# Performance work log

Measured on AMD Instinct MI355X. Metric: run time of the kernel, lower is better.

The kernel has to match this reference:

```python
import jax, jax.numpy as jnp
import numpy as np

EPS = 1e-6

def setup_inputs() -> dict:
    key = jax.random.key(0)
    ks = jax.random.split(key, 8)
    I, S, O = 1024, 512, 1024
    Bsz, T = 4, 2048
    return {
        "u": jax.random.normal(ks[0], (Bsz, T, I), dtype=jnp.float32),
        "dt": jax.random.normal(ks[1], (S,), dtype=jnp.float32),
        "A": jax.random.normal(ks[2], (S,), dtype=jnp.float32),
        "Bmat": jax.random.normal(ks[3], (I, S), dtype=jnp.float32) / np.sqrt(S),
        "C": jax.random.normal(ks[4], (S, O), dtype=jnp.float32) / np.sqrt(S),
        "D": jax.random.normal(ks[5], (O,), dtype=jnp.float32),
        "norm_w": jnp.ones((I,), dtype=jnp.float32),
    }

def _rmsnorm(x, w):
    x32 = x.astype(jnp.float32)
    n = x32 * jax.lax.rsqrt(jnp.mean(x32 * x32, axis=-1, keepdims=True) + EPS)
    return n.astype(x.dtype) * w

def reference(u, dt, A, Bmat, C, D, norm_w):
    u = _rmsnorm(u, norm_w)                      # [B, T, I]
    Bsz, T, _ = u.shape
    dts = jax.nn.sigmoid(dt)                     # [S]
    a = jnp.exp(-dts * jnp.abs(A))               # [S] discretized decay
    t = jnp.arange(T, dtype=jnp.float32)
    h = dts[:, None] * a[:, None] ** t[None, :]  # [S, T] geometric kernel
    u_proj = jnp.einsum('bti,is->bst', u, Bmat)  # [B, S, T]
    # depthwise causal conv: flipped kernel + cross-correlation == convolution
    k = jnp.flip(h, axis=1)[:, None, :]          # [S, 1, T] (OIW)
    x = jax.lax.conv_general_dilated(
        u_proj, k, window_strides=(1,), padding=[(T - 1, T - 1)],
        dimension_numbers=('NCW', 'OIW', 'NCW'),
        feature_group_count=u_proj.shape[1])[:, :, :T]  # [B, S, T]
    x = jnp.transpose(x, (0, 2, 1))              # [B, T, S]
    y = jnp.einsum('bts,so->bto', x, C) + D      # [B, T, O]
    return (y, x[:, -1])
```

## Files before the change

### kernel.cpp

```cpp
#include <hip/hip_runtime.h>
#include <math.h>

#define I_DIM 1024
#define S_DIM 512
#define O_DIM 1024
#define T_DIM 2048
#define B_SZ 4
#define M_ROWS (B_SZ * T_DIM)
#define EPSF 1e-6f

#define CL 64
#define NCH 32

typedef _Float16 f16;
typedef __attribute__((ext_vector_type(8))) _Float16 f16x8;
typedef __attribute__((ext_vector_type(2))) _Float16 f16x2;
typedef __attribute__((ext_vector_type(4))) float f32x4;

__device__ __forceinline__ unsigned short f2h_bits(float f) {
    _Float16 h = (_Float16)f;
    return __builtin_bit_cast(unsigned short, h);
}

__device__ __forceinline__ void load16_lds(const void* g, void* l) {
    __builtin_amdgcn_global_load_lds((const __attribute__((address_space(1))) void*)g,
                                     (__attribute__((address_space(3))) void*)l,
                                     16, 0, 0);
}

__global__ __launch_bounds__(256)
void prep(const float* __restrict__ u, const float* __restrict__ nw,
          unsigned short* __restrict__ u16,
          const float* __restrict__ Bmat, const float* __restrict__ dt,
          unsigned short* __restrict__ Bt16,
          const float* __restrict__ Cmat, unsigned short* __restrict__ Ct16) {
    __shared__ float tile[32][33];
    const int t = threadIdx.x;
    const int bx = blockIdx.x;

    if (bx < M_ROWS) {
        float4 v = ((const float4*)(u + (size_t)bx * I_DIM))[t];
        float ss = v.x * v.x + v.y * v.y + v.z * v.z + v.w * v.w;
        #pragma unroll
        for (int off = 32; off > 0; off >>= 1) ss += __shfl_down(ss, off, 64);
        if ((t & 63) == 0) tile[0][t >> 6] = ss;
        __syncthreads();
        if (t == 0)
            tile[0][0] = rsqrtf((tile[0][0] + tile[0][1] + tile[0][2] + tile[0][3])
                                * (1.0f / I_DIM) + EPSF);
        __syncthreads();
        const float rs = tile[0][0];
        ushort4 o;
        o.x = f2h_bits(v.x * rs);
        o.y = f2h_bits(v.y * rs);
        o.z = f2h_bits(v.z * rs);
        o.w = f2h_bits(v.w * rs);
        ((ushort4*)(u16 + (size_t)bx * I_DIM))[t] = o;
    } else if (bx < M_ROWS + 512) {
        const int tb = bx - M_ROWS;
        const int bs = (tb & 15) * 32;
        const int bi = (tb >> 4) * 32;
        const int tx = t & 31, ty = t >> 5;
        #pragma unroll
        for (int i = ty; i < 32; i += 8)
            tile[i][tx] = Bmat[(size_t)(bi + i) * S_DIM + bs + tx];
        __syncthreads();
        const float w = nw[bi + tx];
        #pragma unroll
        for (int i = ty; i < 32; i += 8) {
            const int s = bs + i;
            const float dts = 1.0f / (1.0f + expf(-dt[s]));
            Bt16[(size_t)s * I_DIM + bi + tx] = f2h_bits(tile[tx][i] * dts * w);
        }
    } else {
        const int tb = bx - M_ROWS - 512;
        const int bo = (tb & 31) * 32;
        const int bs = (tb >> 5) * 32;
        const int tx = t & 31, ty = t >> 5;
        #pragma unroll
        for (int i = ty; i < 32; i += 8)
            tile[i][tx] = Cmat[(size_t)(bs + i) * O_DIM + bo + tx];
        __syncthreads();
        #pragma unroll
        for (int i = ty; i < 32; i += 8)
            Ct16[(size_t)(bo + i) * S_DIM + bs + tx] = f2h_bits(tile[tx][i]);
    }
}

__global__ __launch_bounds__(256)
void gemm1_chfin(const f16* __restrict__ A, const f16* __restrict__ Bt,
                 f16* __restrict__ up, float* __restrict__ chlast,
                 const float* __restrict__ dt, const float* __restrict__ Avec) {
    constexpr int K = I_DIM, N = S_DIM, NK = K / 32;
    __shared__ f16 As[5][64 * 32];
    __shared__ f16 Bs[5][128 * 32];
    const int t = threadIdx.x;

    int bid = blockIdx.x;
    bid = (bid & 7) * 64 + (bid >> 3);
    const int n0 = (bid & 3) * 128;
    const int m0 = (bid >> 2) * 64;
    const int wid = t >> 6, lane = t & 63;
    const int wn = wid * 32, lr = lane & 15, kg = lane >> 4;

    const int swch = (t & 3) ^ ((t >> 3) & 3);
    const f16* aptr = A + (size_t)(m0 + (t >> 2)) * K + swch * 8;
    const f16* bptr = Bt + (size_t)(n0 + (t >> 2)) * K + swch * 8;
    const int rchunk = (kg ^ ((lr >> 1) & 3)) * 8;

    f32x4 acc[4][2];
    #pragma unroll
    for (int i = 0; i < 4; ++i)
        #pragma unroll
        for (int j = 0; j < 2; ++j) acc[i][j] = (f32x4){0.f, 0.f, 0.f, 0.f};

    auto stage = [&](int kt, int slot) {
        load16_lds(aptr + kt * 32, &As[slot][t * 8]);
        load16_lds(bptr + kt * 32, &Bs[slot][t * 8]);
        load16_lds(bptr + (size_t)64 * K + kt * 32, &Bs[slot][2048 + t * 8]);
    };

    stage(0, 0); stage(1, 1); stage(2, 2); stage(3, 3);

    #pragma unroll
    for (int kt = 0; kt < NK; ++kt) {
        if (kt < NK - 3)       asm volatile("s_waitcnt vmcnt(9)");
        else if (kt == NK - 3) asm volatile("s_waitcnt vmcnt(6)");
        else if (kt == NK - 2) asm volatile("s_waitcnt vmcnt(3)");
        else                   asm volatile("s_waitcnt vmcnt(0)");
        __builtin_amdgcn_s_barrier();
        __builtin_amdgcn_sched_barrier(0);
        if (kt + 4 < NK) stage(kt + 4, (kt + 4) % 5);

        const int slot = kt % 5;
        f16x8 af[4], bf[2];
        #pragma unroll
        for (int m = 0; m < 4; ++m)
            af[m] = *(const f16x8*)&As[slot][(m * 16 + lr) * 32 + rchunk];
        #pragma unroll
        for (int n = 0; n < 2; ++n)
            bf[n] = *(const f16x8*)&Bs[slot][(wn + n * 16 + lr) * 32 + rchunk];
        __builtin_amdgcn_s_setprio(1);
        #pragma unroll
        for (int m = 0; m < 4; ++m)
            #pragma unroll
            for (int n = 0; n < 2; ++n)
                acc[m][n] = __builtin_amdgcn_mfma_f32_16x16x32_f16(af[m], bf[n], acc[m][n], 0, 0, 0);
        __builtin_amdgcn_s_setprio(0);
    }

    const int cb = m0 >> 11;
    const int cc = (m0 >> 6) & (NCH - 1);
    #pragma unroll
    for (int n = 0; n < 2; ++n) {
        const int col = n0 + wn + n * 16 + lr;
        const float dts = 1.0f / (1.0f + expf(-dt[col]));
        const float e = dts * fabsf(Avec[col]);
        const float ainv = expf(e);
        float partial = 0.f;
        #pragma unroll
        for (int m = 0; m < 4; ++m) {
            const int row = m * 16 + kg * 4;
            float wgt = expf(-e * (float)(63 - row));
            #pragma unroll
            for (int j = 0; j < 4; ++j) {
                const float val = acc[m][n][j];
                up[(size_t)(m0 + row + j) * N + col] = (_Float16)val;
                partial = fmaf(wgt, val, partial);
                wgt *= ainv;
            }
        }
        partial += __shfl_xor(partial, 16, 64);
        partial += __shfl_xor(partial, 32, 64);
        if (kg == 0)
            chlast[(size_t)(cb * NCH + cc) * S_DIM + col] = partial;
    }
}

__global__ __launch_bounds__(256)
void gemm2_scan(const f16* __restrict__ upb, const float* __restrict__ chlast,
                const f16* __restrict__ Ct, const float* __restrict__ Dvec,
                const float* __restrict__ dt, const float* __restrict__ Avec,
                float* __restrict__ y, float* __restrict__ xlast) {
    constexpr int K = S_DIM, N = O_DIM, NK = K / 32;
    __shared__ __align__(16) unsigned char As[64 * 1024];
    __shared__ f16 Bs[2][128 * 32];
    const int t = threadIdx.x;

    int bid = blockIdx.x;
    bid = (bid & 7) * 128 + (bid >> 3);
    const int n0 = (bid & 7) * 128;
    const int m0 = (bid >> 3) * 64;
    const int wid = t >> 6, lane = t & 63;
    const int wn = wid * 32, lr = lane & 15, kg = lane >> 4;

    const int srcswz = ((t & 3) ^ ((t >> 3) & 3)) * 8;
    const f16* bptr = Ct + (size_t)(n0 + (t >> 2)) * K + srcswz;
    auto stageB = [&](int kt, int slot) {
        load16_lds(bptr + kt * 32, &Bs[slot][t * 8]);
        load16_lds(bptr + (size_t)64 * K + kt * 32, &Bs[slot][2048 + t * 8]);
    };
    stageB(0, 0);
    const int rchunk = (kg ^ ((lr >> 1) & 3)) * 8;

    const unsigned* up32 = (const unsigned*)upb;
    const size_t ub = (size_t)m0 * 256 + t;
    unsigned v[CL];
    #pragma unroll
    for (int j = 0; j < CL; ++j) v[j] = up32[ub + (size_t)j * 256];

    const int cc = (m0 >> 6) & (NCH - 1);
    const int cb = m0 >> 11;
    const int s0 = 2 * t;
    const float dts0 = 1.0f / (1.0f + expf(-dt[s0]));
    const float dts1 = 1.0f / (1.0f + expf(-dt[s0 + 1]));
    const float ab0 = fabsf(Avec[s0]), ab1 = fabsf(Avec[s0 + 1]);
    const float g0 = expf(-dts0 * ab0);
    const float g1 = expf(-dts1 * ab1);
    const float gCL0 = expf(-dts0 * ab0 * (float)CL);
    const float gCL1 = expf(-dts1 * ab1 * (float)CL);
    const float2* ch = (const float2*)chlast;
    float cy0 = 0.f, cy1 = 0.f;
    {
        int j = 0;
        for (; j + 4 <= cc; j += 4) {
            float2 f0 = ch[(size_t)(cb * NCH + j + 0) * 256 + t];
            float2 f1 = ch[(size_t)(cb * NCH + j + 1) * 256 + t];
            float2 f2 = ch[(size_t)(cb * NCH + j + 2) * 256 + t];
            float2 f3 = ch[(size_t)(cb * NCH + j + 3) * 256 + t];
            cy0 = fmaf(gCL0, cy0, f0.x); cy1 = fmaf(gCL1, cy1, f0.y);
            cy0 = fmaf(gCL0, cy0, f1.x); cy1 = fmaf(gCL1, cy1, f1.y);
            cy0 = fmaf(gCL0, cy0, f2.x); cy1 = fmaf(gCL1, cy1, f2.y);
            cy0 = fmaf(gCL0, cy0, f3.x); cy1 = fmaf(gCL1, cy1, f3.y);
        }
        for (; j < cc; ++j) {
            float2 f = ch[(size_t)(cb * NCH + j) * 256 + t];
            cy0 = fmaf(gCL0, cy0, f.x);
            cy1 = fmaf(gCL1, cy1, f.y);
        }
    }

    float x0 = cy0, x1 = cy1;
    #pragma unroll
    for (int j = 0; j < CL; ++j) {
        f16x2 h = __builtin_bit_cast(f16x2, v[j]);
        x0 = fmaf(g0, x0, (float)h.x);
        x1 = fmaf(g1, x1, (float)h.y);
        f16x2 o; o.x = (_Float16)x0; o.y = (_Float16)x1;
        v[j] = __builtin_bit_cast(unsigned, o);
    }
    #pragma unroll
    for (int j = 0; j < CL; ++j)
        *(unsigned*)&As[j * 1024 + ((t * 4) ^ ((j & 7) << 4))] = v[j];
    if (cc == NCH - 1)
        ((float2*)xlast)[cb * 256 + t] = make_float2(x0, x1);
    __syncthreads();

    f32x4 acc[4][2];
    #pragma unroll
    for (int i = 0; i < 4; ++i)
        #pragma unroll
        for (int j = 0; j < 2; ++j) acc[i][j] = (f32x4){0.f, 0.f, 0.f, 0.f};

    const int swz = (lr & 7) << 4;
    for (int kt = 0; kt < NK; ++kt) {
        const int cur = kt & 1;
        if (kt + 1 < NK) {
            stageB(kt + 1, cur ^ 1);
            asm volatile("s_waitcnt vmcnt(2)");
        } else {
            asm volatile("s_waitcnt vmcnt(0)");
        }
        __builtin_amdgcn_s_barrier();
        __builtin_amdgcn_sched_barrier(0);

        f16x8 af[4], bf[2];
        #pragma unroll
        for (int m = 0; m < 4; ++m)
            af[m] = *(const f16x8*)&As[(m * 16 + lr) * 1024 + ((kt * 64 + kg * 16) ^ swz)];
        #pragma unroll
        for (int n = 0; n < 2; ++n)
            bf[n] = *(const f16x8*)&Bs[cur][(wn + n * 16 + lr) * 32 + rchunk];
        __builtin_amdgcn_s_setprio(1);
        #pragma unroll
        for (int m = 0; m < 4; ++m)
            #pragma unroll
            for (int n = 0; n < 2; ++n)
                acc[m][n] = __builtin_amdgcn_mfma_f32_16x16x32_f16(af[m], bf[n], acc[m][n], 0, 0, 0);
        __builtin_amdgcn_s_setprio(0);
        __builtin_amdgcn_s_barrier();
    }

    #pragma unroll
    for (int n = 0; n < 2; ++n) {
        const int col = n0 + wn + n * 16 + lr;
        const float dv = Dvec[col];
        #pragma unroll
        for (int m = 0; m < 4; ++m) {
            const int row = m0 + m * 16 + kg * 4;
            #pragma unroll
            for (int j = 0; j < 4; ++j)
                y[(size_t)(row + j) * N + col] = acc[m][n][j] + dv;
        }
    }
}

extern "C" void kernel_launch(void* const* d_in, const int* in_sizes, int n_in,
                              void* d_out, int out_size, void* d_ws, size_t ws_size,
                              hipStream_t stream) {
    const float* u    = (const float*)d_in[0];
    const float* dt   = (const float*)d_in[1];
    const float* Avec = (const float*)d_in[2];
    const float* Bmat = (const float*)d_in[3];
    const float* Cmat = (const float*)d_in[4];
    const float* Dvec = (const float*)d_in[5];
    const float* nw   = (const float*)d_in[6];

    float* y     = (float*)d_out;
    float* xlast = y + (size_t)M_ROWS * O_DIM;

    char* w = (char*)d_ws;
    unsigned short* u16    = (unsigned short*)(w);
    f16*            up16   = (f16*)(w + 16777216);
    unsigned short* Bt16   = (unsigned short*)(w + 25165824);
    unsigned short* Ct16   = (unsigned short*)(w + 26214400);
    float*          chlast = (float*)(w + 27262976);

    prep<<<M_ROWS + 512 + 512, 256, 0, stream>>>(u, nw, u16, Bmat, dt, Bt16, Cmat, Ct16);

    gemm1_chfin<<<512, 256, 0, stream>>>((const f16*)u16, (const f16*)Bt16,
                                         up16, chlast, dt, Avec);

    gemm2_scan<<<1024, 256, 0, stream>>>(up16, chlast, (const f16*)Ct16, Dvec,
                                         dt, Avec, y, xlast);
}
```

Baseline: 59.28 us.

## Load A tile in two large bursts with XOR swizzle, double-buffer B only

```diff
diff --git a/kernel.cpp b/kernel.cpp
--- a/kernel.cpp
+++ b/kernel.cpp
@@ -91,9 +91,9 @@
 void gemm1_chfin(const f16* __restrict__ A, const f16* __restrict__ Bt,
                  f16* __restrict__ up, float* __restrict__ chlast,
                  const float* __restrict__ dt, const float* __restrict__ Avec) {
-    constexpr int K = I_DIM, N = S_DIM, NK = K / 32;
-    __shared__ f16 As[5][64 * 32];
-    __shared__ f16 Bs[5][128 * 32];
+    constexpr int K = I_DIM, N = S_DIM;
+    __shared__ f16 As[64 * 512];
+    __shared__ f16 Bs[2][128 * 32];
     const int t = threadIdx.x;
 
     int bid = blockIdx.x;
@@ -104,49 +104,67 @@
     const int wn = wid * 32, lr = lane & 15, kg = lane >> 4;
 
     const int swch = (t & 3) ^ ((t >> 3) & 3);
-    const f16* aptr = A + (size_t)(m0 + (t >> 2)) * K + swch * 8;
     const f16* bptr = Bt + (size_t)(n0 + (t >> 2)) * K + swch * 8;
-    const int rchunk = (kg ^ ((lr >> 1) & 3)) * 8;
-
-    f32x4 acc[4][2];
-    #pragma unroll
-    for (int i = 0; i < 4; ++i)
-        #pragma unroll
-        for (int j = 0; j < 2; ++j) acc[i][j] = (f32x4){0.f, 0.f, 0.f, 0.f};
-
-    auto stage = [&](int kt, int slot) {
-        load16_lds(aptr + kt * 32, &As[slot][t * 8]);
+    const int rchunkB = (kg ^ ((lr >> 1) & 3)) * 8;
+    const int axor = lr & 7;
+
+    const int aw = t >> 6;
+    auto burstA = [&](int kh) {
+        #pragma unroll
+        for (int j = 0; j < 16; ++j) {
+            const int row = j * 4 + aw;
+            const int gchk = (t & 63) ^ (row & 7);
+            load16_lds(A + (size_t)(m0 + row) * K + kh * 512 + gchk * 8,
+                       (f16*)As + j * 2048 + t * 8);
+        }
+    };
+    auto stageB = [&](int kt, int slot) {
         load16_lds(bptr + kt * 32, &Bs[slot][t * 8]);
         load16_lds(bptr + (size_t)64 * K + kt * 32, &Bs[slot][2048 + t * 8]);
     };
 
-    stage(0, 0); stage(1, 1); stage(2, 2); stage(3, 3);
-
-    #pragma unroll
-    for (int kt = 0; kt < NK; ++kt) {
-        if (kt < NK - 3)       asm volatile("s_waitcnt vmcnt(9)");
-        else if (kt == NK - 3) asm volatile("s_waitcnt vmcnt(6)");
-        else if (kt == NK - 2) asm volatile("s_waitcnt vmcnt(3)");
-        else                   asm volatile("s_waitcnt vmcnt(0)");
+    f32x4 acc[4][2];
+    #pragma unroll
+    for (int i = 0; i < 4; ++i)
+        #pragma unroll
+        for (int j = 0; j < 2; ++j) acc[i][j] = (f32x4){0.f, 0.f, 0.f, 0.f};
+
+    #pragma unroll
+    for (int kh = 0; kh < 2; ++kh) {
+        burstA(kh);
+        stageB(kh * 16, 0);
+        asm volatile("s_waitcnt vmcnt(0)");
         __builtin_amdgcn_s_barrier();
-        __builtin_amdgcn_sched_barrier(0);
-        if (kt + 4 < NK) stage(kt + 4, (kt + 4) % 5);
-
-        const int slot = kt % 5;
-        f16x8 af[4], bf[2];
-        #pragma unroll
-        for (int m = 0; m < 4; ++m)
-            af[m] = *(const f16x8*)&As[slot][(m * 16 + lr) * 32 + rchunk];
-        #pragma unroll
-        for (int n = 0; n < 2; ++n)
-            bf[n] = *(const f16x8*)&Bs[slot][(wn + n * 16 + lr) * 32 + rchunk];
-        __builtin_amdgcn_s_setprio(1);
-        #pragma unroll
-        for (int m = 0; m < 4; ++m)
+
+        #pragma unroll
+        for (int k = 0; k < 16; ++k) {
+            const int kt = kh * 16 + k;
+            const int cur = k & 1;
+            if (k + 1 < 16) {
+                stageB(kt + 1, cur ^ 1);
+                asm volatile("s_waitcnt vmcnt(2)");
+            } else {
+                asm volatile("s_waitcnt vmcnt(0)");
+            }
+            __builtin_amdgcn_s_barrier();
+            __builtin_amdgcn_sched_barrier(0);
+
+            f16x8 af[4], bf[2];
+            #pragma unroll
+            for (int m = 0; m < 4; ++m)
+                af[m] = *(const f16x8*)&As[(m * 16 + lr) * 512 + (((k * 4 + kg) ^ axor) * 8)];
             #pragma unroll
             for (int n = 0; n < 2; ++n)
-                acc[m][n] = __builtin_amdgcn_mfma_f32_16x16x32_f16(af[m], bf[n], acc[m][n], 0, 0, 0);
-        __builtin_amdgcn_s_setprio(0);
+                bf[n] = *(const f16x8*)&Bs[cur][(wn + n * 16 + lr) * 32 + rchunkB];
+            __builtin_amdgcn_s_setprio(1);
+            #pragma unroll
+            for (int m = 0; m < 4; ++m)
+                #pragma unroll
+                for (int n = 0; n < 2; ++n)
+                    acc[m][n] = __builtin_amdgcn_mfma_f32_16x16x32_f16(af[m], bf[n], acc[m][n], 0, 0, 0);
+            __builtin_amdgcn_s_setprio(0);
+            __builtin_amdgcn_s_barrier();
+        }
     }
 
     const int cb = m0 >> 11;
```

Measured after the change: 59.36 us. Within noise of the previous version (+0.1%).

## Enlarge gemm1 tile to 128x128 with 2x2 warp grid and double buffering

Applied to the files above, without the earlier changes.

```diff
diff --git a/kernel.cpp b/kernel.cpp
--- a/kernel.cpp
+++ b/kernel.cpp
@@ -92,67 +92,71 @@
                  f16* __restrict__ up, float* __restrict__ chlast,
                  const float* __restrict__ dt, const float* __restrict__ Avec) {
     constexpr int K = I_DIM, N = S_DIM, NK = K / 32;
-    __shared__ f16 As[5][64 * 32];
-    __shared__ f16 Bs[5][128 * 32];
+    __shared__ f16 As[2][128 * 32];
+    __shared__ f16 Bs[2][128 * 32];
     const int t = threadIdx.x;
 
     int bid = blockIdx.x;
-    bid = (bid & 7) * 64 + (bid >> 3);
+    bid = (bid & 7) * 32 + (bid >> 3);
     const int n0 = (bid & 3) * 128;
-    const int m0 = (bid >> 2) * 64;
+    const int m0 = (bid >> 2) * 128;
     const int wid = t >> 6, lane = t & 63;
-    const int wn = wid * 32, lr = lane & 15, kg = lane >> 4;
+    const int wm = (wid >> 1) * 64, wn = (wid & 1) * 64;
+    const int lr = lane & 15, kg = lane >> 4;
 
     const int swch = (t & 3) ^ ((t >> 3) & 3);
     const f16* aptr = A + (size_t)(m0 + (t >> 2)) * K + swch * 8;
     const f16* bptr = Bt + (size_t)(n0 + (t >> 2)) * K + swch * 8;
     const int rchunk = (kg ^ ((lr >> 1) & 3)) * 8;
 
-    f32x4 acc[4][2];
+    f32x4 acc[4][4];
     #pragma unroll
     for (int i = 0; i < 4; ++i)
         #pragma unroll
-        for (int j = 0; j < 2; ++j) acc[i][j] = (f32x4){0.f, 0.f, 0.f, 0.f};
+        for (int j = 0; j < 4; ++j) acc[i][j] = (f32x4){0.f, 0.f, 0.f, 0.f};
 
     auto stage = [&](int kt, int slot) {
-        load16_lds(aptr + kt * 32, &As[slot][t * 8]);
-        load16_lds(bptr + kt * 32, &Bs[slot][t * 8]);
-        load16_lds(bptr + (size_t)64 * K + kt * 32, &Bs[slot][2048 + t * 8]);
+        const int k0 = kt * 32;
+        load16_lds(aptr + k0, &As[slot][t * 8]);
+        load16_lds(aptr + (size_t)64 * K + k0, &As[slot][2048 + t * 8]);
+        load16_lds(bptr + k0, &Bs[slot][t * 8]);
+        load16_lds(bptr + (size_t)64 * K + k0, &Bs[slot][2048 + t * 8]);
     };
 
-    stage(0, 0); stage(1, 1); stage(2, 2); stage(3, 3);
-
-    #pragma unroll
+    stage(0, 0);
     for (int kt = 0; kt < NK; ++kt) {
-        if (kt < NK - 3)       asm volatile("s_waitcnt vmcnt(9)");
-        else if (kt == NK - 3) asm volatile("s_waitcnt vmcnt(6)");
-        else if (kt == NK - 2) asm volatile("s_waitcnt vmcnt(3)");
-        else                   asm volatile("s_waitcnt vmcnt(0)");
+        const int cur = kt & 1;
+        if (kt + 1 < NK) {
+            stage(kt + 1, cur ^ 1);
+            asm volatile("s_waitcnt vmcnt(4)");
+        } else {
+            asm volatile("s_waitcnt vmcnt(0)");
+        }
         __builtin_amdgcn_s_barrier();
         __builtin_amdgcn_sched_barrier(0);
-        if (kt + 4 < NK) stage(kt + 4, (kt + 4) % 5);
-
-        const int slot = kt % 5;
-        f16x8 af[4], bf[2];
+
+        f16x8 af[4], bf[4];
         #pragma unroll
         for (int m = 0; m < 4; ++m)
-            af[m] = *(const f16x8*)&As[slot][(m * 16 + lr) * 32 + rchunk];
-        #pragma unroll
-        for (int n = 0; n < 2; ++n)
-            bf[n] = *(const f16x8*)&Bs[slot][(wn + n * 16 + lr) * 32 + rchunk];
+            af[m] = *(const f16x8*)&As[cur][(wm + m * 16 + lr) * 32 + rchunk];
+        #pragma unroll
+        for (int n = 0; n < 4; ++n)
+            bf[n] = *(const f16x8*)&Bs[cur][(wn + n * 16 + lr) * 32 + rchunk];
         __builtin_amdgcn_s_setprio(1);
         #pragma unroll
         for (int m = 0; m < 4; ++m)
             #pragma unroll
-            for (int n = 0; n < 2; ++n)
+            for (int n = 0; n < 4; ++n)
                 acc[m][n] = __builtin_amdgcn_mfma_f32_16x16x32_f16(af[m], bf[n], acc[m][n], 0, 0, 0);
         __builtin_amdgcn_s_setprio(0);
-    }
-
-    const int cb = m0 >> 11;
-    const int cc = (m0 >> 6) & (NCH - 1);
-    #pragma unroll
-    for (int n = 0; n < 2; ++n) {
+        __builtin_amdgcn_s_barrier();
+    }
+
+    const int crow = m0 + wm;
+    const int cb = crow >> 11;
+    const int cc = (crow >> 6) & (NCH - 1);
+    #pragma unroll
+    for (int n = 0; n < 4; ++n) {
         const int col = n0 + wn + n * 16 + lr;
         const float dts = 1.0f / (1.0f + expf(-dt[col]));
         const float e = dts * fabsf(Avec[col]);
@@ -165,7 +169,7 @@
             #pragma unroll
             for (int j = 0; j < 4; ++j) {
                 const float val = acc[m][n][j];
-                up[(size_t)(m0 + row + j) * N + col] = (_Float16)val;
+                up[(size_t)(crow + row + j) * N + col] = (_Float16)val;
                 partial = fmaf(wgt, val, partial);
                 wgt *= ainv;
             }
@@ -328,7 +332,7 @@
 
     prep<<<M_ROWS + 512 + 512, 256, 0, stream>>>(u, nw, u16, Bmat, dt, Bt16, Cmat, Ct16);
 
-    gemm1_chfin<<<512, 256, 0, stream>>>((const f16*)u16, (const f16*)Bt16,
+    gemm1_chfin<<<256, 256, 0, stream>>>((const f16*)u16, (const f16*)Bt16,
                                          up16, chlast, dt, Avec);
 
     gemm2_scan<<<1024, 256, 0, stream>>>(up16, chlast, (const f16*)Ct16, Dvec,
```

New measurement: 67.59 us. 14.0% more time.
